# Kernel optimization log

Hardware: AMD Instinct MI355X
Metric: run time of the kernel (lower is better)

The kernel has to match this reference:

```python
import jax, jax.numpy as jnp
import numpy as np

GLYPH_DIM = 4096
PADDING_IDX = GLYPH_DIM  # 4096
GLYPH_EMB = 20           # CHAR_EMB 16 + COLOR_EMB 4
HIDDEN = 32
MAX_LEN = 64


def setup_inputs() -> dict:
    key = jax.random.key(0)
    k1, k2, k3, k4, k5, k6, k7 = jax.random.split(key, 7)
    B, H, W = 8192, 21, 79
    glyph_chars = jax.random.randint(k1, (B, H, W), 0, 256, dtype=jnp.int32)
    glyph_colors = jax.random.randint(k2, (B, H, W), 0, 16, dtype=jnp.int32)
    # Embedding table with zero padding row (torch padding_idx semantics)
    emb_table = jax.random.normal(k3, (GLYPH_DIM + 1, GLYPH_EMB), dtype=jnp.float32) * 0.02
    emb_table = emb_table.at[PADDING_IDX].set(0.0)
    s = 1.0 / np.sqrt(HIDDEN)
    W_ih = jax.random.uniform(k4, (HIDDEN, GLYPH_EMB), minval=-s, maxval=s, dtype=jnp.float32)
    W_hh = jax.random.uniform(k5, (HIDDEN, HIDDEN), minval=-s, maxval=s, dtype=jnp.float32)
    b_ih = jax.random.uniform(k6, (HIDDEN,), minval=-s, maxval=s, dtype=jnp.float32)
    b_hh = jax.random.uniform(k7, (HIDDEN,), minval=-s, maxval=s, dtype=jnp.float32)
    return {"glyph_chars": glyph_chars, "glyph_colors": glyph_colors,
            "emb_table": emb_table, "W_ih": W_ih, "W_hh": W_hh,
            "b_ih": b_ih, "b_hh": b_hh}


def _encode_bag(glyph_chars, glyph_colors):
    """Batched sorted-unique compaction over the bounded glyph id range."""
    B = glyph_chars.shape[0]
    g_ids = ((glyph_chars << 4) + glyph_colors).reshape(B, -1)  # [B, H*W]
    # presence[b, g] = glyph g appears in sample b (batched histogram)
    bidx = jnp.broadcast_to(jnp.arange(B, dtype=g_ids.dtype)[:, None], g_ids.shape)
    presence = jnp.zeros((B, GLYPH_DIM), dtype=bool).at[bidx, g_ids].set(True)
    # compact: present ids keep their value, absent become PADDING_IDX (=4096),
    # so sorting yields ascending unique ids followed by padding.
    ids = jnp.arange(GLYPH_DIM, dtype=jnp.int32)
    keys = jnp.where(presence, ids, jnp.int32(PADDING_IDX))
    bag = jnp.sort(keys, axis=1)[:, :MAX_LEN]  # [B, MAX_LEN]
    lengths = jnp.minimum(presence.sum(axis=1), MAX_LEN)  # [B]
    return bag, lengths


def reference(glyph_chars, glyph_colors, emb_table, W_ih, W_hh, b_ih, b_hh):
    bag, lengths = _encode_bag(glyph_chars, glyph_colors)
    emb = emb_table[bag]  # [B, MAX_LEN, GLYPH_EMB]
    B = emb.shape[0]

    # packed RNN == plain RNN where hidden state freezes past each sequence length
    xs = jnp.swapaxes(emb, 0, 1)  # [T, B, E]

    def step(h, inp):
        xt, t = inp
        h_new = jnp.tanh(xt @ W_ih.T + b_ih + h @ W_hh.T + b_hh)
        h = jnp.where((t < lengths)[:, None], h_new, h)
        return h, None

    h0 = jnp.zeros((B, HIDDEN), dtype=emb.dtype)
    h, _ = jax.lax.scan(step, h0, (xs, jnp.arange(MAX_LEN)))
    return (h, emb, bag)
```

## Files before the change

kernel.cpp:

```cpp
#include <hip/hip_runtime.h>

#define HW 1659
#define PADID 4096
#define EMB 20
#define HID 32
#define MAXLEN 64

__global__ __launch_bounds__(256) void bag_emb_kernel(
    const int* __restrict__ chars, const int* __restrict__ colors,
    const float* __restrict__ emb_table,
    float* __restrict__ out_emb, float* __restrict__ out_bag)
{
    __shared__ unsigned bm[128];
    __shared__ int sc[128];
    __shared__ int bagl[64];

    const int b = blockIdx.x;
    const int tid = threadIdx.x;

    if (tid < 128) bm[tid] = 0u;
    if (tid < 64) bagl[tid] = PADID;
    __syncthreads();

    const int base = b * HW;
    for (int i = tid; i < HW; i += 256) {
        int g = (chars[base + i] << 4) + colors[base + i];
        atomicOr(&bm[g >> 5], 1u << (g & 31));
    }
    __syncthreads();

    int cnt = 0;
    if (tid < 128) { cnt = __popc(bm[tid]); sc[tid] = cnt; }
    __syncthreads();
    for (int d = 1; d < 128; d <<= 1) {
        int v = 0;
        if (tid >= d && tid < 128) v = sc[tid - d];
        __syncthreads();
        if (tid < 128) sc[tid] += v;
        __syncthreads();
    }

    if (tid < 128) {
        unsigned w = bm[tid];
        int p = sc[tid] - cnt;
        while (w && p < 64) {
            int bit = __ffs(w) - 1;
            bagl[p++] = (tid << 5) | bit;
            w &= w - 1;
        }
    }
    __syncthreads();

    if (tid < 64) out_bag[(size_t)b * 64 + tid] = (float)bagl[tid];

    const float4* tab4 = (const float4*)emb_table;
    float4* dst4 = (float4*)(out_emb + (size_t)b * (MAXLEN * EMB));
    for (int q = tid; q < MAXLEN * 5; q += 256) {
        int t = q / 5;
        int m = q - t * 5;
        int row = bagl[t];
        dst4[q] = tab4[row * 5 + m];
    }
}

__global__ __launch_bounds__(256, 4) void rnn_kernel(
    const float* __restrict__ emb, const float* __restrict__ bagf,
    const float* __restrict__ W_ih, const float* __restrict__ W_hh,
    const float* __restrict__ b_ih, const float* __restrict__ b_hh,
    float* __restrict__ out_h)
{
    __shared__ float hbuf[2][8][36];

    const int tid = threadIdx.x;
    const int ib  = tid >> 5;
    const int j   = tid & 31;
    const int b   = blockIdx.x * 8 + ib;

    float wih[EMB];
#pragma unroll
    for (int k = 0; k < EMB; k++) wih[k] = W_ih[j * EMB + k];
    float whh[HID];
#pragma unroll
    for (int k = 0; k < HID; k++) whh[k] = W_hh[j * HID + k];
    const float sbias = b_ih[j] + b_hh[j];

    const float* bp = bagf + (size_t)b * 64;
    unsigned long long m0 = __ballot(bp[j]      < 4095.5f);
    unsigned long long m1 = __ballot(bp[32 + j] < 4095.5f);
    const int half = ib & 1;
    const int len = __popc((unsigned)(m0 >> (half * 32)))
                  + __popc((unsigned)(m1 >> (half * 32)));

    hbuf[0][ib][j] = 0.f;
    float h = 0.f;
    const float* xb = emb + (size_t)b * (MAXLEN * EMB);

    __syncthreads();

    int cur = 0;
    for (int t = 0; t < MAXLEN; t++) {
        float4 x0 = ((const float4*)(xb + t * EMB))[0];
        float4 x1 = ((const float4*)(xb + t * EMB))[1];
        float4 x2 = ((const float4*)(xb + t * EMB))[2];
        float4 x3 = ((const float4*)(xb + t * EMB))[3];
        float4 x4 = ((const float4*)(xb + t * EMB))[4];

        float s = sbias;
        const float4* hb4 = (const float4*)hbuf[cur][ib];
#pragma unroll
        for (int m = 0; m < 8; m++) {
            float4 hv = hb4[m];
            s += whh[4*m+0]*hv.x + whh[4*m+1]*hv.y
               + whh[4*m+2]*hv.z + whh[4*m+3]*hv.w;
        }
        s += wih[0]*x0.x + wih[1]*x0.y + wih[2]*x0.z + wih[3]*x0.w;
        s += wih[4]*x1.x + wih[5]*x1.y + wih[6]*x1.z + wih[7]*x1.w;
        s += wih[8]*x2.x + wih[9]*x2.y + wih[10]*x2.z + wih[11]*x2.w;
        s += wih[12]*x3.x + wih[13]*x3.y + wih[14]*x3.z + wih[15]*x3.w;
        s += wih[16]*x4.x + wih[17]*x4.y + wih[18]*x4.z + wih[19]*x4.w;

        s = fminf(fmaxf(s, -9.f), 9.f);
        float e = __expf(2.f * s);
        float th = (e - 1.f) * __builtin_amdgcn_rcpf(e + 1.f);

        h = (t < len) ? th : h;

        hbuf[cur ^ 1][ib][j] = h;
        __syncthreads();
        cur ^= 1;
    }

    out_h[(size_t)b * HID + j] = h;
}

extern "C" void kernel_launch(void* const* d_in, const int* in_sizes, int n_in,
                              void* d_out, int out_size, void* d_ws, size_t ws_size,
                              hipStream_t stream) {
    const int*   chars     = (const int*)d_in[0];
    const int*   colors    = (const int*)d_in[1];
    const float* emb_table = (const float*)d_in[2];
    const float* W_ih      = (const float*)d_in[3];
    const float* W_hh      = (const float*)d_in[4];
    const float* b_ih      = (const float*)d_in[5];
    const float* b_hh      = (const float*)d_in[6];

    const int B = in_sizes[0] / HW;

    float* out     = (float*)d_out;
    float* out_h   = out;
    float* out_emb = out + (size_t)B * HID;
    float* out_bag = out_emb + (size_t)B * MAXLEN * EMB;

    bag_emb_kernel<<<B, 256, 0, stream>>>(chars, colors, emb_table, out_emb, out_bag);
    rnn_kernel<<<B / 8, 256, 0, stream>>>(out_emb, out_bag, W_ih, W_hh, b_ih, b_hh, out_h);
}
```

Before: 211.5 us.

## Drop block barriers in RNN and rebuild bag compaction without LDS atomics

The bag kernel now marks glyph presence with plain byte stores into a 4096-byte shared array, replacing atomicOr on a bitmap. It reads chars and colors with aligned int4 loads and computes the prefix sum with wave64 shuffles plus a small cross-wave sum, instead of a barrier-heavy shared-memory scan. The RNN kernel switches to 128-thread blocks and a single hidden-state buffer per sample, and replaces the per-step __syncthreads with an LDS waitcnt. That relies on each sample's 32 lanes sitting inside one wave64 and running in lockstep. Empty asm constraints keep the weights pinned in registers. The cost is a dependence on wave-level execution semantics in place of explicit synchronisation.

After: 198.8 us. 6.0% less time.

```diff
diff --git a/kernel.cpp b/kernel.cpp
--- a/kernel.cpp
+++ b/kernel.cpp
@@ -11,42 +11,70 @@
     const float* __restrict__ emb_table,
     float* __restrict__ out_emb, float* __restrict__ out_bag)
 {
-    __shared__ unsigned bm[128];
-    __shared__ int sc[128];
+    __shared__ unsigned char pres[4096];
     __shared__ int bagl[64];
+    __shared__ int wsum[4];
 
-    const int b = blockIdx.x;
+    const int b   = blockIdx.x;
     const int tid = threadIdx.x;
+    const int lane = tid & 63;
+    const int wv   = tid >> 6;
 
-    if (tid < 128) bm[tid] = 0u;
+    ((uint4*)pres)[tid] = make_uint4(0u, 0u, 0u, 0u);
     if (tid < 64) bagl[tid] = PADID;
     __syncthreads();
 
     const int base = b * HW;
-    for (int i = tid; i < HW; i += 256) {
-        int g = (chars[base + i] << 4) + colors[base + i];
-        atomicOr(&bm[g >> 5], 1u << (g & 31));
+    const int pe = (4 - (base & 3)) & 3;
+    if (tid < pe) {
+        int g = (chars[base + tid] << 4) + colors[base + tid];
+        pres[g] = 1;
+    }
+    const int nv = (HW - pe) >> 2;
+    const int nt = HW - pe - (nv << 2);
+    const int4* c4 = (const int4*)(chars + base + pe);
+    const int4* k4 = (const int4*)(colors + base + pe);
+    for (int v = tid; v < nv; v += 256) {
+        int4 c = c4[v], k = k4[v];
+        pres[(c.x << 4) + k.x] = 1;
+        pres[(c.y << 4) + k.y] = 1;
+        pres[(c.z << 4) + k.z] = 1;
+        pres[(c.w << 4) + k.w] = 1;
+    }
+    if (tid < nt) {
+        int i = base + pe + (nv << 2) + tid;
+        int g = (chars[i] << 4) + colors[i];
+        pres[g] = 1;
     }
     __syncthreads();
 
-    int cnt = 0;
-    if (tid < 128) { cnt = __popc(bm[tid]); sc[tid] = cnt; }
+    uint4 w4 = ((const uint4*)pres)[tid];
+    const unsigned M = 0x01010101u;
+    int cnt = __popc(w4.x & M) + __popc(w4.y & M)
+            + __popc(w4.z & M) + __popc(w4.w & M);
+
+    int pre = cnt;
+#pragma unroll
+    for (int d = 1; d < 64; d <<= 1) {
+        int v = __shfl_up(pre, d, 64);
+        if (lane >= d) pre += v;
+    }
+    if (lane == 63) wsum[wv] = pre;
     __syncthreads();
-    for (int d = 1; d < 128; d <<= 1) {
-        int v = 0;
-        if (tid >= d && tid < 128) v = sc[tid - d];
-        __syncthreads();
-        if (tid < 128) sc[tid] += v;
-        __syncthreads();
-    }
+    int wbase = 0;
+#pragma unroll
+    for (int w2 = 0; w2 < 4; w2++) wbase += (w2 < wv) ? wsum[w2] : 0;
+    int p = wbase + pre - cnt;
 
-    if (tid < 128) {
-        unsigned w = bm[tid];
-        int p = sc[tid] - cnt;
-        while (w && p < 64) {
-            int bit = __ffs(w) - 1;
-            bagl[p++] = (tid << 5) | bit;
-            w &= w - 1;
+    unsigned wrd[4] = {w4.x, w4.y, w4.z, w4.w};
+#pragma unroll
+    for (int c = 0; c < 4; c++) {
+#pragma unroll
+        for (int k = 0; k < 4; k++) {
+            if ((wrd[c] >> (8 * k)) & 1) {
+                if (p < 64) bagl[p] = 16 * tid + 4 * c + k;
+                p++;
+            }
         }
     }
     __syncthreads();
@@ -63,18 +91,18 @@
     }
 }
 
-__global__ __launch_bounds__(256, 4) void rnn_kernel(
+__global__ __launch_bounds__(128, 4) void rnn_kernel(
     const float* __restrict__ emb, const float* __restrict__ bagf,
     const float* __restrict__ W_ih, const float* __restrict__ W_hh,
     const float* __restrict__ b_ih, const float* __restrict__ b_hh,
     float* __restrict__ out_h)
 {
-    __shared__ float hbuf[2][8][36];
+    __shared__ float hbuf[4][32];
 
     const int tid = threadIdx.x;
     const int ib  = tid >> 5;
     const int j   = tid & 31;
-    const int b   = blockIdx.x * 8 + ib;
+    const int b   = blockIdx.x * 4 + ib;
 
     float wih[EMB];
 #pragma unroll
@@ -82,6 +110,10 @@
     float whh[HID];
 #pragma unroll
     for (int k = 0; k < HID; k++) whh[k] = W_hh[j * HID + k];
+#pragma unroll
+    for (int k = 0; k < EMB; k++) asm("" : "+v"(wih[k]));
+#pragma unroll
+    for (int k = 0; k < HID; k++) asm("" : "+v"(whh[k]));
     const float sbias = b_ih[j] + b_hh[j];
 
     const float* bp = bagf + (size_t)b * 64;
@@ -91,22 +123,18 @@
     const int len = __popc((unsigned)(m0 >> (half * 32)))
                   + __popc((unsigned)(m1 >> (half * 32)));
 
-    hbuf[0][ib][j] = 0.f;
+    hbuf[ib][j] = 0.f;
+    asm volatile("s_waitcnt lgkmcnt(0)" ::: "memory");
+
     float h = 0.f;
     const float* xb = emb + (size_t)b * (MAXLEN * EMB);
 
-    __syncthreads();
-
-    int cur = 0;
     for (int t = 0; t < MAXLEN; t++) {
-        float4 x0 = ((const float4*)(xb + t * EMB))[0];
-        float4 x1 = ((const float4*)(xb + t * EMB))[1];
-        float4 x2 = ((const float4*)(xb + t * EMB))[2];
-        float4 x3 = ((const float4*)(xb + t * EMB))[3];
-        float4 x4 = ((const float4*)(xb + t * EMB))[4];
+        const float4* xp = (const float4*)(xb + t * EMB);
+        float4 x0 = xp[0], x1 = xp[1], x2 = xp[2], x3 = xp[3], x4 = xp[4];
 
         float s = sbias;
-        const float4* hb4 = (const float4*)hbuf[cur][ib];
+        const float4* hb4 = (const float4*)hbuf[ib];
 #pragma unroll
         for (int m = 0; m < 8; m++) {
             float4 hv = hb4[m];
@@ -125,9 +153,8 @@
 
         h = (t < len) ? th : h;
 
-        hbuf[cur ^ 1][ib][j] = h;
-        __syncthreads();
-        cur ^= 1;
+        hbuf[ib][j] = h;
+        asm volatile("s_waitcnt lgkmcnt(0)" ::: "memory");
     }
 
     out_h[(size_t)b * HID + j] = h;
@@ -152,5 +179,5 @@
     float* out_bag = out_emb + (size_t)B * MAXLEN * EMB;
 
     bag_emb_kernel<<<B, 256, 0, stream>>>(chars, colors, emb_table, out_emb, out_bag);
-    rnn_kernel<<<B / 8, 256, 0, stream>>>(out_emb, out_bag, W_ih, W_hh, b_ih, b_hh, out_h);
+    rnn_kernel<<<B / 4, 128, 0, stream>>>(out_emb, out_bag, W_ih, W_hh, b_ih, b_hh, out_h);
 }
```
